# Performance work log

Hardware: AMD Instinct MI355X
Metric: run time of the kernel (lower is better)

The kernel has to match this reference:

```python
import jax, jax.numpy as jnp
import numpy as np

N_NODES = 20000
N_EDGES = 320000
N_GRAPHS = 512
VOCAB = 32
D = 256
K_HOPS = 4
EPS = 1e-5


def setup_inputs() -> dict:
    key = jax.random.key(0)
    ks = jax.random.split(key, 16)
    s = 0.02
    return {
        "x": jax.random.randint(ks[0], (N_NODES,), 0, VOCAB),
        "edge_index": jax.random.randint(ks[1], (2, N_EDGES), 0, N_NODES),
        "batch": jnp.sort(jax.random.randint(ks[2], (N_NODES,), 0, N_GRAPHS)),
        "node_table": jax.random.normal(ks[3], (VOCAB, D)) * s,
        "sg_W": jax.random.normal(ks[4], (D, D)) * s,
        "sg_b": jnp.zeros((D,)),
        "W1": jax.random.normal(ks[5], (D, 2 * D)) * s,
        "b1": jnp.zeros((2 * D,)),
        "g1": jnp.ones((2 * D,)),
        "be1": jnp.zeros((2 * D,)),
        "W2": jax.random.normal(ks[6], (2 * D, D)) * s,
        "b2": jnp.zeros((D,)),
        "g2": jnp.ones((D,)),
        "be2": jnp.zeros((D,)),
        "W3": jax.random.normal(ks[7], (D, 1)) * s,
        "b3": jnp.zeros((1,)),
    }


def _batchnorm(z, g, b):
    # BatchNorm1d in training-mode math (batch statistics), deterministic.
    m = z.mean(axis=0)
    v = z.var(axis=0)
    return (z - m) * jax.lax.rsqrt(v + EPS) * g + b


def reference(x, edge_index, batch, node_table, sg_W, sg_b,
              W1, b1, g1, be1, W2, b2, g2, be2, W3, b3):
    n = node_table.shape[0] and x.shape[0]  # N nodes
    h = node_table[x]  # [N, D] node embedding lookup (NodeEncoder)

    # SGConv: add self-loops, symmetric normalization, K hops, then Linear.
    loop = jnp.arange(n, dtype=edge_index.dtype)
    src = jnp.concatenate([edge_index[0], loop])
    dst = jnp.concatenate([edge_index[1], loop])
    deg = jax.ops.segment_sum(jnp.ones_like(dst, dtype=h.dtype), dst, num_segments=n)
    dinv = jnp.where(deg > 0, jax.lax.rsqrt(jnp.maximum(deg, 1.0)), 0.0)
    norm = (dinv[src] * dinv[dst])[:, None]  # [E+N, 1]
    for _ in range(K_HOPS):
        h = jax.ops.segment_sum(h[src] * norm, dst, num_segments=n)
    h = h @ sg_W + sg_b  # [N, D]

    # global_add_pool over graphs (dropout = identity in eval)
    hg = jax.ops.segment_sum(h, batch, num_segments=N_GRAPHS)  # [G, D]

    hg = jax.nn.relu(_batchnorm(hg @ W1 + b1, g1, be1))  # [G, 2D]
    hg = jax.nn.relu(_batchnorm(hg @ W2 + b2, g2, be2))  # [G, D]
    return hg @ W3 + b3  # [G, num_tasks]
```

## Files before the change

kernel.cpp:

```cpp
#include <hip/hip_runtime.h>

#define N_NODES  20000
#define N_EDGES  320000
#define N_GRAPHS 512
#define VOCAB    32
#define D        256
#define TWO_D    512
#define EPS      1e-5f
#define CAP      64
#define HB       (N_NODES / 16)


__global__ __launch_bounds__(256) void zero_kernel(int* __restrict__ cnt,
                                                   float* __restrict__ cs1,
                                                   float* __restrict__ cs2) {
    int i = blockIdx.x * 256 + threadIdx.x;
    if (i < N_NODES) cnt[i] = 0;
    if (i < 2 * TWO_D) cs1[i] = 0.f;
    if (i < 2 * D) cs2[i] = 0.f;
}


__global__ __launch_bounds__(256) void bucket_kernel(const int* __restrict__ src,
                                                     const int* __restrict__ dst,
                                                     int* __restrict__ cnt,
                                                     int* __restrict__ buckets) {
    int e = blockIdx.x * 256 + threadIdx.x;
    if (e >= N_EDGES) return;
    int d = dst[e];
    int slot = atomicAdd(&cnt[d], 1);
    if (slot < CAP) buckets[d * CAP + slot] = src[e];
}


__global__ __launch_bounds__(256) void prep_kernel(const int* __restrict__ x,
                                                   const int* __restrict__ batch,
                                                   const int* __restrict__ cnt,
                                                   float* __restrict__ q,
                                                   float* __restrict__ rdinv,
                                                   float* __restrict__ r0,
                                                   int* __restrict__ gstart) {
    int node = (blockIdx.x << 4) | (threadIdx.x >> 4);
    int sub = threadIdx.x & 15;
    int c = cnt[node];
    float dinv = rsqrtf((float)(c + 1));
    if (sub == 0) {
        q[node]     = 1.f / (float)(c + 1);
        rdinv[node] = sqrtf((float)(c + 1));
    }
    int xf = x[node];
    int f0 = sub * 2;
    ((float2*)r0)[node * 16 + sub] =
        make_float2(xf == f0 ? dinv : 0.f, xf == f0 + 1 ? dinv : 0.f);

    int i = blockIdx.x * 256 + threadIdx.x;
    if (i < N_NODES) {
        int b = batch[i];
        if (i == 0) { for (int g = 0; g <= b; ++g) gstart[g] = 0; }
        else { int pb = batch[i - 1]; for (int g = pb + 1; g <= b; ++g) gstart[g] = i; }
        if (i == N_NODES - 1) { for (int g = b + 1; g <= N_GRAPHS; ++g) gstart[g] = N_NODES; }
    }
}


__global__ __launch_bounds__(512) void foldG_kernel(const float* __restrict__ table,
                                                    const float* __restrict__ sgW,
                                                    const float* __restrict__ sg_b,
                                                    const float* __restrict__ W1,
                                                    float* __restrict__ G,
                                                    float* __restrict__ u) {
    int r = blockIdx.x;
    int j = threadIdx.x;
    __shared__ float trow[D];
    __shared__ float frow[D];
    if (r < VOCAB) {
        if (j < D) trow[j] = table[r * D + j];
        __syncthreads();
        if (j < D) {
            float acc = 0.f;
            for (int k = 0; k < D; ++k) acc += trow[k] * sgW[k * D + j];
            frow[j] = acc;
        }
    } else {
        if (j < D) frow[j] = sg_b[j];
    }
    __syncthreads();
    float acc = 0.f;
    for (int k = 0; k < D; ++k) acc += frow[k] * W1[k * TWO_D + j];
    float* dst = (r < VOCAB) ? (G + r * TWO_D) : u;
    dst[j] = acc;
}


__global__ __launch_bounds__(256) void hop_kernel(const float* __restrict__ rin,
                                                  float* __restrict__ rout,
                                                  const int* __restrict__ cnt,
                                                  const int* __restrict__ buckets,
                                                  const float* __restrict__ q) {
    int node = (blockIdx.x << 4) | (threadIdx.x >> 4);
    int sub = threadIdx.x & 15;
    const float2* M2 = (const float2*)rin;
    float2 self = M2[node * 16 + sub];
    float ax = self.x, ay = self.y;
    float bx = 0.f, by = 0.f, cx = 0.f, cy = 0.f, dx = 0.f, dy = 0.f;
    int n = min(cnt[node], CAP);
    const int* bk = buckets + node * CAP;
    int j = 0;
    for (; j + 4 <= n; j += 4) {
        int s0 = bk[j], s1 = bk[j + 1], s2 = bk[j + 2], s3 = bk[j + 3];
        float2 v0 = M2[s0 * 16 + sub], v1 = M2[s1 * 16 + sub];
        float2 v2 = M2[s2 * 16 + sub], v3 = M2[s3 * 16 + sub];
        ax += v0.x; ay += v0.y;
        bx += v1.x; by += v1.y;
        cx += v2.x; cy += v2.y;
        dx += v3.x; dy += v3.y;
    }
    for (; j < n; ++j) {
        int s = bk[j];
        float2 v = M2[s * 16 + sub];
        ax += v.x; ay += v.y;
    }
    float qd = q[node];
    ((float2*)rout)[node * 16 + sub] =
        make_float2(qd * (ax + bx + cx + dx), qd * (ay + by + cy + dy));
}


__global__ __launch_bounds__(256) void lin1p_kernel(const float* __restrict__ M,
                                                    const float* __restrict__ rdinv,
                                                    const int* __restrict__ gstart,
                                                    const float* __restrict__ G,
                                                    const float* __restrict__ u,
                                                    const float* __restrict__ b1,
                                                    float* __restrict__ z1,
                                                    float* __restrict__ cs1) {
    __shared__ float S[8 * VOCAB];
    __shared__ float gcnt[8];
    int g0 = blockIdx.x * 8;
    int tid = threadIdx.x;
    int grp = tid >> 5, f = tid & 31;
    int g = g0 + grp;
    int lo = gstart[g], hi = gstart[g + 1];
    float s = 0.f;
    for (int i = lo; i < hi; ++i) s += M[i * 32 + f] * rdinv[i];
    S[grp * 32 + f] = s;
    if (f == 0) gcnt[grp] = (float)(hi - lo);
    __syncthreads();
    float a0[8], a1[8];
#pragma unroll
    for (int i = 0; i < 8; ++i) { a0[i] = 0.f; a1[i] = 0.f; }
    for (int k = 0; k < VOCAB; ++k) {
        float w0 = G[k * TWO_D + tid];
        float w1 = G[k * TWO_D + tid + 256];
#pragma unroll
        for (int i = 0; i < 8; ++i) {
            float r = S[i * VOCAB + k];
            a0[i] += r * w0; a1[i] += r * w1;
        }
    }
    float u0 = u[tid], u1 = u[tid + 256];
    float c0 = b1[tid], c1 = b1[tid + 256];
    float s0 = 0.f, ss0 = 0.f, s1 = 0.f, ss1 = 0.f;
#pragma unroll
    for (int i = 0; i < 8; ++i) {
        float gc = gcnt[i];
        float z0v = a0[i] + gc * u0 + c0;
        float z1v = a1[i] + gc * u1 + c1;
        z1[(g0 + i) * TWO_D + tid]       = z0v;
        z1[(g0 + i) * TWO_D + tid + 256] = z1v;
        s0 += z0v; ss0 += z0v * z0v;
        s1 += z1v; ss1 += z1v * z1v;
    }
    atomicAdd(&cs1[tid], s0);
    atomicAdd(&cs1[TWO_D + tid], ss0);
    atomicAdd(&cs1[tid + 256], s1);
    atomicAdd(&cs1[TWO_D + tid + 256], ss1);
}


__global__ __launch_bounds__(256) void lin2_kernel(const float* __restrict__ z1,
                                                   const float* __restrict__ cs1,
                                                   const float* __restrict__ g1,
                                                   const float* __restrict__ be1,
                                                   const float* __restrict__ W2,
                                                   const float* __restrict__ b2,
                                                   float* __restrict__ z2,
                                                   float* __restrict__ cs2) {
    __shared__ float A[TWO_D], C[TWO_D];
    __shared__ float rows[4 * TWO_D];
    int tid = threadIdx.x;
    int g0 = blockIdx.x * 4;
    for (int k = tid; k < TWO_D; k += 256) {
        float m = cs1[k] * (1.f / N_GRAPHS);
        float var = cs1[TWO_D + k] * (1.f / N_GRAPHS) - m * m;
        float a = rsqrtf(var + EPS) * g1[k];
        A[k] = a;
        C[k] = be1[k] - m * a;
    }
    __syncthreads();
    for (int idx = tid; idx < 4 * TWO_D; idx += 256) {
        int k = idx & (TWO_D - 1);
        float v = z1[g0 * TWO_D + idx] * A[k] + C[k];
        rows[idx] = v > 0.f ? v : 0.f;
    }
    __syncthreads();
    float acc[4] = {0.f, 0.f, 0.f, 0.f};
    for (int k = 0; k < TWO_D; ++k) {
        float wv = W2[k * D + tid];
        acc[0] += rows[k] * wv;
        acc[1] += rows[TWO_D + k] * wv;
        acc[2] += rows[2 * TWO_D + k] * wv;
        acc[3] += rows[3 * TWO_D + k] * wv;
    }
    float bb = b2[tid];
    float s = 0.f, ss = 0.f;
#pragma unroll
    for (int i = 0; i < 4; ++i) {
        float zv = acc[i] + bb;
        z2[(g0 + i) * D + tid] = zv;
        s += zv; ss += zv * zv;
    }
    atomicAdd(&cs2[tid], s);
    atomicAdd(&cs2[D + tid], ss);
}


__global__ __launch_bounds__(64) void head_kernel(const float* __restrict__ z2,
                                                  const float* __restrict__ cs2,
                                                  const float* __restrict__ g2,
                                                  const float* __restrict__ be2,
                                                  const float* __restrict__ W3,
                                                  const float* __restrict__ b3,
                                                  float* __restrict__ out) {
    __shared__ float A[D], C[D];
    int g = blockIdx.x;
    int lane = threadIdx.x;
    for (int k = lane; k < D; k += 64) {
        float m = cs2[k] * (1.f / N_GRAPHS);
        float var = cs2[D + k] * (1.f / N_GRAPHS) - m * m;
        float a = rsqrtf(var + EPS) * g2[k];
        A[k] = a;
        C[k] = be2[k] - m * a;
    }
    __syncthreads();
    float acc = 0.f;
    for (int k = lane; k < D; k += 64) {
        float v = z2[g * D + k] * A[k] + C[k];
        v = v > 0.f ? v : 0.f;
        acc += v * W3[k];
    }
    for (int off = 32; off; off >>= 1) acc += __shfl_down(acc, off);
    if (lane == 0) out[g] = acc + b3[0];
}


extern "C" void kernel_launch(void* const* d_in, const int* in_sizes, int n_in,
                              void* d_out, int out_size, void* d_ws, size_t ws_size,
                              hipStream_t stream) {
    const int*   x     = (const int*)d_in[0];
    const int*   e_src = (const int*)d_in[1];
    const int*   e_dst = (const int*)d_in[1] + N_EDGES;
    const int*   batch = (const int*)d_in[2];
    const float* table = (const float*)d_in[3];
    const float* sg_W  = (const float*)d_in[4];
    const float* sg_b  = (const float*)d_in[5];
    const float* W1    = (const float*)d_in[6];
    const float* b1    = (const float*)d_in[7];
    const float* g1    = (const float*)d_in[8];
    const float* be1   = (const float*)d_in[9];
    const float* W2    = (const float*)d_in[10];
    const float* b2    = (const float*)d_in[11];
    const float* g2    = (const float*)d_in[12];
    const float* be2   = (const float*)d_in[13];
    const float* W3    = (const float*)d_in[14];
    const float* b3    = (const float*)d_in[15];
    float*       out   = (float*)d_out;

    char* p = (char*)d_ws;
    auto alloc = [&](size_t bytes) { char* q = p; p += (bytes + 15) & ~size_t(15); return q; };
    float* m_a     = (float*)alloc((size_t)N_NODES * VOCAB * 4);
    float* m_b     = (float*)alloc((size_t)N_NODES * VOCAB * 4);
    int*   cnt     = (int*)  alloc((size_t)N_NODES * 4);
    int*   buckets = (int*)  alloc((size_t)N_NODES * CAP * 4);
    float* q       = (float*)alloc((size_t)N_NODES * 4);
    float* rdinv   = (float*)alloc((size_t)N_NODES * 4);
    int*   gstart  = (int*)  alloc((size_t)(N_GRAPHS + 1) * 4);
    float* G       = (float*)alloc((size_t)VOCAB * TWO_D * 4);
    float* u       = (float*)alloc((size_t)TWO_D * 4);
    float* z1      = (float*)alloc((size_t)N_GRAPHS * TWO_D * 4);
    float* z2      = (float*)alloc((size_t)N_GRAPHS * D * 4);
    float* cs1     = (float*)alloc((size_t)2 * TWO_D * 4);
    float* cs2     = (float*)alloc((size_t)2 * D * 4);

    zero_kernel<<<(N_NODES + 255) / 256, 256, 0, stream>>>(cnt, cs1, cs2);
    bucket_kernel<<<(N_EDGES + 255) / 256, 256, 0, stream>>>(e_src, e_dst, cnt, buckets);
    prep_kernel<<<HB, 256, 0, stream>>>(x, batch, cnt, q, rdinv, m_a, gstart);
    foldG_kernel<<<VOCAB + 1, 512, 0, stream>>>(table, sg_W, sg_b, W1, G, u);

    hop_kernel<<<HB, 256, 0, stream>>>(m_a, m_b, cnt, buckets, q);
    hop_kernel<<<HB, 256, 0, stream>>>(m_b, m_a, cnt, buckets, q);
    hop_kernel<<<HB, 256, 0, stream>>>(m_a, m_b, cnt, buckets, q);
    hop_kernel<<<HB, 256, 0, stream>>>(m_b, m_a, cnt, buckets, q);

    lin1p_kernel<<<N_GRAPHS / 8, 256, 0, stream>>>(m_a, rdinv, gstart, G, u, b1, z1, cs1);
    lin2_kernel<<<N_GRAPHS / 4, 256, 0, stream>>>(z1, cs1, g1, be1, W2, b2, z2, cs2);
    head_kernel<<<N_GRAPHS, 64, 0, stream>>>(z2, cs2, g2, be2, W3, b3, out);
}
```

Baseline: 136.7 us.

## Store hop state in bf16, fuse zero/fold kernels, and fold prep into first hop

The per-node 32-wide hop state is now stored as packed bf16 pairs instead of fp32, halving gather traffic in the hop kernels. The zeroing, gstart construction and the G/u weight-folding kernels are merged into one launch, and the prep kernel is removed: the first hop builds the one-hot input on the fly from x and cnt. Scale factors q and rdinv are recomputed from cnt rather than stored. Rounding to bf16 across four hops reduces accuracy of the propagated features.

```diff
diff --git a/kernel.cpp b/kernel.cpp
--- a/kernel.cpp
+++ b/kernel.cpp
@@ -11,13 +11,61 @@
 #define HB       (N_NODES / 16)
 
 
-__global__ __launch_bounds__(256) void zero_kernel(int* __restrict__ cnt,
-                                                   float* __restrict__ cs1,
-                                                   float* __restrict__ cs2) {
-    int i = blockIdx.x * 256 + threadIdx.x;
-    if (i < N_NODES) cnt[i] = 0;
-    if (i < 2 * TWO_D) cs1[i] = 0.f;
-    if (i < 2 * D) cs2[i] = 0.f;
+__device__ __forceinline__ unsigned int pack_bf2(float a, float b) {
+    unsigned int ua = __float_as_uint(a);
+    unsigned int ub = __float_as_uint(b);
+    ua = (ua + 0x7FFFu + ((ua >> 16) & 1u)) >> 16;
+    ub = (ub + 0x7FFFu + ((ub >> 16) & 1u)) >> 16;
+    return ua | (ub << 16);
+}
+__device__ __forceinline__ float bf_lo(unsigned int v) { return __uint_as_float(v << 16); }
+__device__ __forceinline__ float bf_hi(unsigned int v) { return __uint_as_float(v & 0xFFFF0000u); }
+
+
+__global__ __launch_bounds__(512) void zero_fold_kernel(const int* __restrict__ batch,
+                                                        int* __restrict__ cnt,
+                                                        float* __restrict__ cs1,
+                                                        float* __restrict__ cs2,
+                                                        int* __restrict__ gstart,
+                                                        const float* __restrict__ table,
+                                                        const float* __restrict__ sgW,
+                                                        const float* __restrict__ sg_b,
+                                                        const float* __restrict__ W1,
+                                                        float* __restrict__ G,
+                                                        float* __restrict__ u) {
+    __shared__ float trow[D];
+    __shared__ float frow[D];
+    int bid = blockIdx.x, tid = threadIdx.x;
+    if (bid < 40) {
+        int i = bid * 512 + tid;
+        if (i < N_NODES) {
+            cnt[i] = 0;
+            int b = batch[i];
+            if (i == 0) { for (int g = 0; g <= b; ++g) gstart[g] = 0; }
+            else { int pb = batch[i - 1]; for (int g = pb + 1; g <= b; ++g) gstart[g] = i; }
+            if (i == N_NODES - 1) { for (int g = b + 1; g <= N_GRAPHS; ++g) gstart[g] = N_NODES; }
+        }
+        if (i < 2 * TWO_D) cs1[i] = 0.f;
+        if (i < 2 * D) cs2[i] = 0.f;
+    } else {
+        int r = bid - 40;
+        if (r < VOCAB) {
+            if (tid < D) trow[tid] = table[r * D + tid];
+            __syncthreads();
+            if (tid < D) {
+                float acc = 0.f;
+                for (int k = 0; k < D; ++k) acc += trow[k] * sgW[k * D + tid];
+                frow[tid] = acc;
+            }
+        } else {
+            if (tid < D) frow[tid] = sg_b[tid];
+        }
+        __syncthreads();
+        float acc = 0.f;
+        for (int k = 0; k < D; ++k) acc += frow[k] * W1[k * TWO_D + tid];
+        float* dst = (r < VOCAB) ? (G + r * TWO_D) : u;
+        dst[tid] = acc;
+    }
 }
 
 
@@ -33,101 +81,77 @@
 }
 
 
-__global__ __launch_bounds__(256) void prep_kernel(const int* __restrict__ x,
-                                                   const int* __restrict__ batch,
+__global__ __launch_bounds__(256) void hop1_kernel(const int* __restrict__ x,
                                                    const int* __restrict__ cnt,
-                                                   float* __restrict__ q,
-                                                   float* __restrict__ rdinv,
-                                                   float* __restrict__ r0,
-                                                   int* __restrict__ gstart) {
+                                                   const int* __restrict__ buckets,
+                                                   unsigned int* __restrict__ rout) {
     int node = (blockIdx.x << 4) | (threadIdx.x >> 4);
     int sub = threadIdx.x & 15;
-    int c = cnt[node];
-    float dinv = rsqrtf((float)(c + 1));
-    if (sub == 0) {
-        q[node]     = 1.f / (float)(c + 1);
-        rdinv[node] = sqrtf((float)(c + 1));
-    }
+    int f0 = sub * 2, f1 = f0 + 1;
+    int cd = cnt[node];
+    float dn = rsqrtf((float)(cd + 1));
     int xf = x[node];
-    int f0 = sub * 2;
-    ((float2*)r0)[node * 16 + sub] =
-        make_float2(xf == f0 ? dinv : 0.f, xf == f0 + 1 ? dinv : 0.f);
-
-    int i = blockIdx.x * 256 + threadIdx.x;
-    if (i < N_NODES) {
-        int b = batch[i];
-        if (i == 0) { for (int g = 0; g <= b; ++g) gstart[g] = 0; }
-        else { int pb = batch[i - 1]; for (int g = pb + 1; g <= b; ++g) gstart[g] = i; }
-        if (i == N_NODES - 1) { for (int g = b + 1; g <= N_GRAPHS; ++g) gstart[g] = N_NODES; }
-    }
-}
-
-
-__global__ __launch_bounds__(512) void foldG_kernel(const float* __restrict__ table,
-                                                    const float* __restrict__ sgW,
-                                                    const float* __restrict__ sg_b,
-                                                    const float* __restrict__ W1,
-                                                    float* __restrict__ G,
-                                                    float* __restrict__ u) {
-    int r = blockIdx.x;
-    int j = threadIdx.x;
-    __shared__ float trow[D];
-    __shared__ float frow[D];
-    if (r < VOCAB) {
-        if (j < D) trow[j] = table[r * D + j];
-        __syncthreads();
-        if (j < D) {
-            float acc = 0.f;
-            for (int k = 0; k < D; ++k) acc += trow[k] * sgW[k * D + j];
-            frow[j] = acc;
-        }
-    } else {
-        if (j < D) frow[j] = sg_b[j];
-    }
-    __syncthreads();
-    float acc = 0.f;
-    for (int k = 0; k < D; ++k) acc += frow[k] * W1[k * TWO_D + j];
-    float* dst = (r < VOCAB) ? (G + r * TWO_D) : u;
-    dst[j] = acc;
-}
-
-
-__global__ __launch_bounds__(256) void hop_kernel(const float* __restrict__ rin,
-                                                  float* __restrict__ rout,
+    float ax = (xf == f0) ? dn : 0.f;
+    float ay = (xf == f1) ? dn : 0.f;
+    float bx = 0.f, by = 0.f;
+    int n = min(cd, CAP);
+    const int* bk = buckets + node * CAP;
+    int j = 0;
+    for (; j + 2 <= n; j += 2) {
+        int s0 = bk[j], s1 = bk[j + 1];
+        int xs0 = x[s0], xs1 = x[s1];
+        float d0 = rsqrtf((float)(cnt[s0] + 1));
+        float d1 = rsqrtf((float)(cnt[s1] + 1));
+        ax += (xs0 == f0) ? d0 : 0.f;
+        ay += (xs0 == f1) ? d0 : 0.f;
+        bx += (xs1 == f0) ? d1 : 0.f;
+        by += (xs1 == f1) ? d1 : 0.f;
+    }
+    if (j < n) {
+        int s0 = bk[j];
+        int xs0 = x[s0];
+        float d0 = rsqrtf((float)(cnt[s0] + 1));
+        ax += (xs0 == f0) ? d0 : 0.f;
+        ay += (xs0 == f1) ? d0 : 0.f;
+    }
+    float q = 1.f / (float)(cd + 1);
+    rout[node * 16 + sub] = pack_bf2(q * (ax + bx), q * (ay + by));
+}
+
+
+__global__ __launch_bounds__(256) void hop_kernel(const unsigned int* __restrict__ rin,
+                                                  unsigned int* __restrict__ rout,
                                                   const int* __restrict__ cnt,
-                                                  const int* __restrict__ buckets,
-                                                  const float* __restrict__ q) {
+                                                  const int* __restrict__ buckets) {
     int node = (blockIdx.x << 4) | (threadIdx.x >> 4);
     int sub = threadIdx.x & 15;
-    const float2* M2 = (const float2*)rin;
-    float2 self = M2[node * 16 + sub];
-    float ax = self.x, ay = self.y;
+    int cd = cnt[node];
+    unsigned int self = rin[node * 16 + sub];
+    float ax = bf_lo(self), ay = bf_hi(self);
     float bx = 0.f, by = 0.f, cx = 0.f, cy = 0.f, dx = 0.f, dy = 0.f;
-    int n = min(cnt[node], CAP);
+    int n = min(cd, CAP);
     const int* bk = buckets + node * CAP;
     int j = 0;
     for (; j + 4 <= n; j += 4) {
         int s0 = bk[j], s1 = bk[j + 1], s2 = bk[j + 2], s3 = bk[j + 3];
-        float2 v0 = M2[s0 * 16 + sub], v1 = M2[s1 * 16 + sub];
-        float2 v2 = M2[s2 * 16 + sub], v3 = M2[s3 * 16 + sub];
-        ax += v0.x; ay += v0.y;
-        bx += v1.x; by += v1.y;
-        cx += v2.x; cy += v2.y;
-        dx += v3.x; dy += v3.y;
+        unsigned int v0 = rin[s0 * 16 + sub], v1 = rin[s1 * 16 + sub];
+        unsigned int v2 = rin[s2 * 16 + sub], v3 = rin[s3 * 16 + sub];
+        ax += bf_lo(v0); ay += bf_hi(v0);
+        bx += bf_lo(v1); by += bf_hi(v1);
+        cx += bf_lo(v2); cy += bf_hi(v2);
+        dx += bf_lo(v3); dy += bf_hi(v3);
     }
     for (; j < n; ++j) {
-        int s = bk[j];
-        float2 v = M2[s * 16 + sub];
-        ax += v.x; ay += v.y;
-    }
-    float qd = q[node];
-    ((float2*)rout)[node * 16 + sub] =
-        make_float2(qd * (ax + bx + cx + dx), qd * (ay + by + cy + dy));
-}
-
-
-__global__ __launch_bounds__(256) void lin1p_kernel(const float* __restrict__ M,
-                                                    const float* __restrict__ rdinv,
+        unsigned int v = rin[bk[j] * 16 + sub];
+        ax += bf_lo(v); ay += bf_hi(v);
+    }
+    float q = 1.f / (float)(cd + 1);
+    rout[node * 16 + sub] = pack_bf2(q * (ax + bx + cx + dx), q * (ay + by + cy + dy));
+}
+
+
+__global__ __launch_bounds__(256) void lin1p_kernel(const unsigned int* __restrict__ M,
+                                                    const int* __restrict__ cnt,
                                                     const int* __restrict__ gstart,
                                                     const float* __restrict__ G,
                                                     const float* __restrict__ u,
@@ -142,7 +166,11 @@
     int g = g0 + grp;
     int lo = gstart[g], hi = gstart[g + 1];
     float s = 0.f;
-    for (int i = lo; i < hi; ++i) s += M[i * 32 + f] * rdinv[i];
+    for (int i = lo; i < hi; ++i) {
+        unsigned int v = M[i * 16 + (f >> 1)];
+        float rv = sqrtf((float)(cnt[i] + 1));
+        s += ((f & 1) ? bf_hi(v) : bf_lo(v)) * rv;
+    }
     S[grp * 32 + f] = s;
     if (f == 0) gcnt[grp] = (float)(hi - lo);
     __syncthreads();
@@ -278,12 +306,10 @@
 
     char* p = (char*)d_ws;
     auto alloc = [&](size_t bytes) { char* q = p; p += (bytes + 15) & ~size_t(15); return q; };
-    float* m_a     = (float*)alloc((size_t)N_NODES * VOCAB * 4);
-    float* m_b     = (float*)alloc((size_t)N_NODES * VOCAB * 4);
+    unsigned int* m_a = (unsigned int*)alloc((size_t)N_NODES * 16 * 4);
+    unsigned int* m_b = (unsigned int*)alloc((size_t)N_NODES * 16 * 4);
     int*   cnt     = (int*)  alloc((size_t)N_NODES * 4);
     int*   buckets = (int*)  alloc((size_t)N_NODES * CAP * 4);
-    float* q       = (float*)alloc((size_t)N_NODES * 4);
-    float* rdinv   = (float*)alloc((size_t)N_NODES * 4);
     int*   gstart  = (int*)  alloc((size_t)(N_GRAPHS + 1) * 4);
     float* G       = (float*)alloc((size_t)VOCAB * TWO_D * 4);
     float* u       = (float*)alloc((size_t)TWO_D * 4);
@@ -292,17 +318,16 @@
     float* cs1     = (float*)alloc((size_t)2 * TWO_D * 4);
     float* cs2     = (float*)alloc((size_t)2 * D * 4);
 
-    zero_kernel<<<(N_NODES + 255) / 256, 256, 0, stream>>>(cnt, cs1, cs2);
+    zero_fold_kernel<<<73, 512, 0, stream>>>(batch, cnt, cs1, cs2, gstart,
+                                             table, sg_W, sg_b, W1, G, u);
     bucket_kernel<<<(N_EDGES + 255) / 256, 256, 0, stream>>>(e_src, e_dst, cnt, buckets);
-    prep_kernel<<<HB, 256, 0, stream>>>(x, batch, cnt, q, rdinv, m_a, gstart);
-    foldG_kernel<<<VOCAB + 1, 512, 0, stream>>>(table, sg_W, sg_b, W1, G, u);
-
-    hop_kernel<<<HB, 256, 0, stream>>>(m_a, m_b, cnt, buckets, q);
-    hop_kernel<<<HB, 256, 0, stream>>>(m_b, m_a, cnt, buckets, q);
-    hop_kernel<<<HB, 256, 0, stream>>>(m_a, m_b, cnt, buckets, q);
-    hop_kernel<<<HB, 256, 0, stream>>>(m_b, m_a, cnt, buckets, q);
-
-    lin1p_kernel<<<N_GRAPHS / 8, 256, 0, stream>>>(m_a, rdinv, gstart, G, u, b1, z1, cs1);
+
+    hop1_kernel<<<HB, 256, 0, stream>>>(x, cnt, buckets, m_b);
+    hop_kernel <<<HB, 256, 0, stream>>>(m_b, m_a, cnt, buckets);
+    hop_kernel <<<HB, 256, 0, stream>>>(m_a, m_b, cnt, buckets);
+    hop_kernel <<<HB, 256, 0, stream>>>(m_b, m_a, cnt, buckets);
+
+    lin1p_kernel<<<N_GRAPHS / 8, 256, 0, stream>>>(m_a, cnt, gstart, G, u, b1, z1, cs1);
     lin2_kernel<<<N_GRAPHS / 4, 256, 0, stream>>>(z1, cs1, g1, be1, W2, b2, z2, cs2);
     head_kernel<<<N_GRAPHS, 64, 0, stream>>>(z2, cs2, g2, be2, W3, b3, out);
 }
```

Measured after the change: 120.8 us. 11.6% less time.
